# Performance work log

Measured on AMD Instinct MI355X. Metric: run time of the kernel, lower is better.

## Reference

```python
import jax, jax.numpy as jnp
from jax import lax
import numpy as np

H = 256  # hidden_size


def gru_last(x, Wih, Whh, bih, bhh):
    """Single-layer torch-convention GRU; returns last hidden state.
    x: [B, T, C] -> [B, H]"""
    B, T, _ = x.shape
    h_dim = Whh.shape[1]
    xW = x @ Wih.T + bih  # [B, T, 3H], precompute input gates
    def step(h, xw):
        gi_r, gi_z, gi_n = jnp.split(xw, 3, axis=-1)
        gh = h @ Whh.T + bhh
        gh_r, gh_z, gh_n = jnp.split(gh, 3, axis=-1)
        r = jax.nn.sigmoid(gi_r + gh_r)
        z = jax.nn.sigmoid(gi_z + gh_z)
        n = jnp.tanh(gi_n + r * gh_n)
        return (1.0 - z) * n + z * h, None
    h0 = jnp.zeros((B, h_dim), x.dtype)
    hT, _ = lax.scan(step, h0, jnp.swapaxes(xW, 0, 1))
    return hT


def setup_inputs() -> dict:
    key = jax.random.key(0)
    ks = jax.random.split(key, 16)
    B, N, M, C, C1 = 32, 64, 64, 64, 16
    inter = 2 * H + 6 * C + C1  # 912
    s = 0.05
    x1 = jax.random.normal(ks[0], (B, N, C1), jnp.float32)
    states = jax.random.normal(ks[1], (B, N, M, C), jnp.float32)
    perm1 = jax.vmap(lambda k: jax.random.permutation(k, M))(jax.random.split(ks[2], N)).astype(jnp.int64)
    perm2 = jax.vmap(lambda k: jax.random.permutation(k, N))(jax.random.split(ks[3], N)).astype(jnp.int64)
    return {
        "x1": x1, "states": states, "perm1": perm1, "perm2": perm2,
        # shared 2D->1D GRU (ModuleList([gru]*2) shares parameters)
        "gru2d_Wih": jax.random.normal(ks[4], (3 * H, C), jnp.float32) * s,
        "gru2d_Whh": jax.random.normal(ks[5], (3 * H, H), jnp.float32) * s,
        "gru2d_bih": jax.random.normal(ks[6], (3 * H,), jnp.float32) * s,
        "gru2d_bhh": jax.random.normal(ks[7], (3 * H,), jnp.float32) * s,
        "gru1d_Wih": jax.random.normal(ks[8], (3 * H, inter), jnp.float32) * s,
        "gru1d_Whh": jax.random.normal(ks[9], (3 * H, H), jnp.float32) * s,
        "gru1d_bih": jax.random.normal(ks[10], (3 * H,), jnp.float32) * s,
        "gru1d_bhh": jax.random.normal(ks[11], (3 * H,), jnp.float32) * s,
        "fc1_W": jax.random.normal(ks[12], (H, 3 * inter + H), jnp.float32) * s,
        "fc1_b": jax.random.normal(ks[13], (H,), jnp.float32) * s,
        "fc2_W": jax.random.normal(ks[14], (1, H), jnp.float32) * s,
        "fc2_b": jax.random.normal(ks[15], (1,), jnp.float32) * s,
    }


def reference(x1, states, perm1, perm2,
              gru2d_Wih, gru2d_Whh, gru2d_bih, gru2d_bhh,
              gru1d_Wih, gru1d_Whh, gru1d_bih, gru1d_bhh,
              fc1_W, fc1_b, fc2_W, fc2_b):
    B, N, M, C = states.shape
    d = [states.max(1), states.mean(1), states.min(1),   # [B, M, C] each (N==M)
         states.max(2), states.mean(2), states.min(2)]   # [B, N, C] each
    idx = jnp.arange(N)[:, None]
    # g1[b,i,t,c] = states[b, i, perm1[i,t], c]
    g1 = states[:, idx, perm1, :]                         # [B, N, M, C]
    # g2[b,i,t,c] = states[b, perm2[i,t], i, c]
    g2 = states[:, perm2, idx, :]                         # [B, N, N, C]
    sd1 = gru_last(g1.reshape(B * N, M, C), gru2d_Wih, gru2d_Whh, gru2d_bih, gru2d_bhh).reshape(B, N, H)
    sd2 = gru_last(g2.reshape(B * N, N, C), gru2d_Wih, gru2d_Whh, gru2d_bih, gru2d_bhh).reshape(B, N, H)
    f = jnp.concatenate(d + [sd1, sd2], axis=2)           # [B, N, 6C + 2H]
    f = jnp.concatenate([x1, f], axis=-1)                 # [B, N, inter]
    hlast = gru_last(f, gru1d_Wih, gru1d_Whh, gru1d_bih, gru1d_bhh)  # [B, H]
    g = jnp.concatenate([f.max(1), f.mean(1), f.min(1), hlast], axis=1)
    h = jax.nn.relu(g @ fc1_W.T + fc1_b)
    out = h @ fc2_W.T + fc2_b
    return out.reshape(B)
```

## Files before the change

kernel.cpp:

```cpp
#include <hip/hip_runtime.h>
#include <cmath>

#define B_ 32
#define N_ 64
#define H_ 256
#define G3_ 768
#define INTER_ 912
#define KP_ 928
#define FCIN_ 2992

#define PADA 264
#define PADX 72

typedef __attribute__((ext_vector_type(8))) short short8;
typedef __attribute__((ext_vector_type(4))) short sshort4;
typedef __attribute__((ext_vector_type(4))) float float4v;

#define MFMA __builtin_amdgcn_mfma_f32_16x16x32_bf16

__device__ __forceinline__ float sigmoid_f(float x) {
    return __builtin_amdgcn_rcpf(1.0f + __builtin_amdgcn_exp2f(-1.44269504f * x));
}
__device__ __forceinline__ float tanh_fast(float x) {
    return 1.0f - 2.0f * __builtin_amdgcn_rcpf(1.0f + __builtin_amdgcn_exp2f(2.88539008f * x));
}
__device__ __forceinline__ unsigned f2bf_bits(float x) {
    unsigned u = __float_as_uint(x);
    return (u + 0x7fffu + ((u >> 16) & 1u)) >> 16;
}
__device__ __forceinline__ short f2bf(float x) { return (short)f2bf_bits(x); }

__global__ __launch_bounds__(256) void prep_kernel(
        const float* __restrict__ Whh2, const float* __restrict__ Wih2,
        const float* __restrict__ Whh1, const float* __restrict__ Wih1,
        const float* __restrict__ fc1W,
        short* __restrict__ Bfrag, short* __restrict__ Bfrag1,
        short* __restrict__ Bfrag1W, float* __restrict__ fc1Wt) {
    int idx = blockIdx.x * 256 + threadIdx.x;
    if (idx < 10 * 48 * 64 * 8) {
        int j = idx & 7, lane = (idx >> 3) & 63, tile = idx >> 9;
        int nt = tile % 48, kt = tile / 48;
        int n = nt * 16 + (lane & 15);
        int kb = (lane >> 4) * 8 + j;
        float v = (kt < 8) ? Whh2[n * 256 + kt * 32 + kb]
                           : Wih2[n * 64 + (kt - 8) * 32 + kb];
        Bfrag[idx] = f2bf(v);
    }
    if (idx < 8 * 48 * 64 * 8) {
        int j = idx & 7, lane = (idx >> 3) & 63, tile = idx >> 9;
        int nt = tile % 48, kt = tile / 48;
        int n = nt * 16 + (lane & 15);
        int k = kt * 32 + (lane >> 4) * 8 + j;
        Bfrag1[idx] = f2bf(Whh1[n * 256 + k]);
    }
    if (idx < 29 * 48 * 64 * 8) {
        int j = idx & 7, lane = (idx >> 3) & 63, tile = idx >> 9;
        int nt = tile % 48, kt = tile / 48;
        int n = nt * 16 + (lane & 15);
        int k = kt * 32 + (lane >> 4) * 8 + j;
        Bfrag1W[idx] = (k < INTER_) ? f2bf(Wih1[n * INTER_ + k]) : (short)0;
    }
    if (idx < FCIN_ * 256) {
        int o = idx & 255, i = idx >> 8;
        fc1Wt[idx] = fc1W[o * FCIN_ + i];
    }
}

__global__ __launch_bounds__(256) void reduce_states_kernel(
        const float* __restrict__ states, const float* __restrict__ x1,
        float* __restrict__ f) {
    const int c = threadIdx.x & 63;
    const int bj = blockIdx.x * 4 + (threadIdx.x >> 6);
    const int b = bj >> 6, j = bj & 63;
    const float* p1 = states + b * 262144 + j * 64 + c;
    const float* p2 = states + b * 262144 + j * 4096 + c;
    float mx1 = -1e30f, mn1 = 1e30f, sm1 = 0.f;
    float mx2 = -1e30f, mn2 = 1e30f, sm2 = 0.f;
    #pragma unroll 8
    for (int n = 0; n < 64; ++n) {
        float v = p1[n * 4096];
        mx1 = fmaxf(mx1, v); mn1 = fminf(mn1, v); sm1 += v;
    }
    #pragma unroll 8
    for (int m = 0; m < 64; ++m) {
        float v = p2[m * 64];
        mx2 = fmaxf(mx2, v); mn2 = fminf(mn2, v); sm2 += v;
    }
    float* fr = f + bj * INTER_;
    fr[16 + c]  = mx1;  fr[80 + c]  = sm1 * (1.f / 64.f);  fr[144 + c] = mn1;
    fr[208 + c] = mx2;  fr[272 + c] = sm2 * (1.f / 64.f);  fr[336 + c] = mn2;
    if (c < 16) fr[c] = x1[bj * 16 + c];
}

__global__ __launch_bounds__(512, 1) void gru2d_mfma(
        const float* __restrict__ states,
        const int* __restrict__ perm1, const int* __restrict__ perm2,
        const short* __restrict__ Bfrag,
        const float* __restrict__ bih, const float* __restrict__ bhh,
        float* __restrict__ f) {
    __shared__ short hA[2][16 * PADA];
    __shared__ short xA[2][16 * PADX];
    __shared__ short8 Blds[2 * 48 * 64];
    __shared__ int perms[1024];

    const int tid = threadIdx.x;
    const int lane = tid & 63;
    const int w = tid >> 6;
    const int m = lane & 15;
    const int q = lane >> 4;
    const bool sd2 = blockIdx.x >= 128;
    const int sblock = (blockIdx.x & 127) * 16;

    for (int i = tid; i < 1024; i += 512) {
        int r = i >> 6, t = i & 63;
        int qq = (sblock + r) & 63;
        perms[i] = sd2 ? perm2[qq * 64 + t] : perm1[qq * 64 + t];
    }
    for (int i = tid; i < 16 * PADA; i += 512) hA[0][i] = 0;
    {
        const uint4* src = (const uint4*)(Bfrag + 6 * 48 * 64 * 8);
        uint4* dst = (uint4*)Blds;
        #pragma unroll
        for (int rep = 0; rep < 12; ++rep)
            dst[tid + rep * 512] = src[tid + rep * 512];
    }

    const short8* Bf8 = (const short8*)Bfrag;
    short8 Bres[36];
    #pragma unroll
    for (int kt = 0; kt < 6; ++kt)
        #pragma unroll
        for (int j = 0; j < 6; ++j)
            Bres[kt * 6 + j] = Bf8[(kt * 48 + 8 * j + w) * 64 + lane];

    const int u0 = 16 * w + m;
    const int u1 = 128 + u0;
    const float br0 = bih[u0] + bhh[u0],             br1 = bih[u1] + bhh[u1];
    const float bz0 = bih[256 + u0] + bhh[256 + u0], bz1 = bih[256 + u1] + bhh[256 + u1];
    const float bnx0 = bih[512 + u0], bnx1 = bih[512 + u1];
    const float bnh0 = bhh[512 + u0], bnh1 = bhh[512 + u1];

    float4v hreg0 = {0.f, 0.f, 0.f, 0.f}, hreg1 = {0.f, 0.f, 0.f, 0.f};

    {
        #pragma unroll
        for (int half = 0; half < 2; ++half) {
            int i = tid + half * 512;
            int r = i >> 6, c = i & 63;
            int s = sblock + r, b = s >> 6, qq = s & 63;
            int p = perms[r * 64 + 0];
            int src = sd2 ? ((b * 64 + p) * 64 + qq) * 64 + c
                          : ((b * 64 + qq) * 64 + p) * 64 + c;
            xA[0][r * PADX + c] = f2bf(states[src]);
        }
    }
    __syncthreads();

    for (int t = 0; t < 64; ++t) {
        const short* hAc = hA[t & 1];
        const short* xAc = xA[t & 1];

        short8 Bx[12];
        #pragma unroll
        for (int kt = 0; kt < 2; ++kt)
            #pragma unroll
            for (int j = 0; j < 6; ++j)
                Bx[kt * 6 + j] = Bf8[((8 + kt) * 48 + 8 * j + w) * 64 + lane];

        float xg0 = 0.f, xg1 = 0.f;
        int w0 = -1, w1 = -1;
        if (t + 1 < 64) {
            #pragma unroll
            for (int half = 0; half < 2; ++half) {
                int i = tid + half * 512;
                int r = i >> 6, c = i & 63;
                int s = sblock + r, b = s >> 6, qq = s & 63;
                int p = perms[r * 64 + t + 1];
                int src = sd2 ? ((b * 64 + p) * 64 + qq) * 64 + c
                              : ((b * 64 + qq) * 64 + p) * 64 + c;
                float v = states[src];
                if (half == 0) { xg0 = v; w0 = r * PADX + c; }
                else           { xg1 = v; w1 = r * PADX + c; }
            }
        }

        float4v aR0 = {br0, br0, br0, br0},     aR1 = {br1, br1, br1, br1};
        float4v aZ0 = {bz0, bz0, bz0, bz0},     aZ1 = {bz1, bz1, bz1, bz1};
        float4v aNh0 = {bnh0, bnh0, bnh0, bnh0}, aNh1 = {bnh1, bnh1, bnh1, bnh1};
        float4v aNx0 = {bnx0, bnx0, bnx0, bnx0}, aNx1 = {bnx1, bnx1, bnx1, bnx1};

        #pragma unroll
        for (int kt = 0; kt < 6; ++kt) {
            short8 a = *(const short8*)(hAc + m * PADA + kt * 32 + q * 8);
            aR0  = MFMA(a, Bres[kt * 6 + 0], aR0, 0, 0, 0);
            aR1  = MFMA(a, Bres[kt * 6 + 1], aR1, 0, 0, 0);
            aZ0  = MFMA(a, Bres[kt * 6 + 2], aZ0, 0, 0, 0);
            aZ1  = MFMA(a, Bres[kt * 6 + 3], aZ1, 0, 0, 0);
            aNh0 = MFMA(a, Bres[kt * 6 + 4], aNh0, 0, 0, 0);
            aNh1 = MFMA(a, Bres[kt * 6 + 5], aNh1, 0, 0, 0);
        }
        #pragma unroll
        for (int kt = 0; kt < 2; ++kt) {
            short8 a = *(const short8*)(hAc + m * PADA + (6 + kt) * 32 + q * 8);
            short8 b0 = Blds[(kt * 48 + 8 * 0 + w) * 64 + lane];
            short8 b1 = Blds[(kt * 48 + 8 * 1 + w) * 64 + lane];
            short8 b2 = Blds[(kt * 48 + 8 * 2 + w) * 64 + lane];
            short8 b3 = Blds[(kt * 48 + 8 * 3 + w) * 64 + lane];
            short8 b4 = Blds[(kt * 48 + 8 * 4 + w) * 64 + lane];
            short8 b5 = Blds[(kt * 48 + 8 * 5 + w) * 64 + lane];
            aR0  = MFMA(a, b0, aR0, 0, 0, 0);
            aR1  = MFMA(a, b1, aR1, 0, 0, 0);
            aZ0  = MFMA(a, b2, aZ0, 0, 0, 0);
            aZ1  = MFMA(a, b3, aZ1, 0, 0, 0);
            aNh0 = MFMA(a, b4, aNh0, 0, 0, 0);
            aNh1 = MFMA(a, b5, aNh1, 0, 0, 0);
        }
        #pragma unroll
        for (int kt = 0; kt < 2; ++kt) {
            short8 a = *(const short8*)(xAc + m * PADX + kt * 32 + q * 8);
            aR0  = MFMA(a, Bx[kt * 6 + 0], aR0, 0, 0, 0);
            aR1  = MFMA(a, Bx[kt * 6 + 1], aR1, 0, 0, 0);
            aZ0  = MFMA(a, Bx[kt * 6 + 2], aZ0, 0, 0, 0);
            aZ1  = MFMA(a, Bx[kt * 6 + 3], aZ1, 0, 0, 0);
            aNx0 = MFMA(a, Bx[kt * 6 + 4], aNx0, 0, 0, 0);
            aNx1 = MFMA(a, Bx[kt * 6 + 5], aNx1, 0, 0, 0);
        }

        short* hAn = hA[(t + 1) & 1];
        #pragma unroll
        for (int p = 0; p < 4; ++p) {
            int row = q * 4 + p;
            float r0 = sigmoid_f(aR0[p]);
            float z0 = sigmoid_f(aZ0[p]);
            float n0 = tanh_fast(aNx0[p] + r0 * aNh0[p]);
            float h0 = n0 + z0 * (hreg0[p] - n0);
            hreg0[p] = h0;
            hAn[row * PADA + u0] = f2bf(h0);
            float r1 = sigmoid_f(aR1[p]);
            float z1 = sigmoid_f(aZ1[p]);
            float n1 = tanh_fast(aNx1[p] + r1 * aNh1[p]);
            float h1 = n1 + z1 * (hreg1[p] - n1);
            hreg1[p] = h1;
            hAn[row * PADA + u1] = f2bf(h1);
        }
        if (t + 1 < 64) {
            xA[(t + 1) & 1][w0] = f2bf(xg0);
            xA[(t + 1) & 1][w1] = f2bf(xg1);
        }
        __syncthreads();
    }

    const int off = sd2 ? 656 : 400;
    #pragma unroll
    for (int p = 0; p < 4; ++p) {
        int s = sblock + q * 4 + p;
        f[s * INTER_ + off + u0] = hreg0[p];
        f[s * INTER_ + off + u1] = hreg1[p];
    }
}

__global__ __launch_bounds__(256) void convert_f_kernel(
        const float* __restrict__ f, short* __restrict__ fbf) {
    int idx = blockIdx.x * 256 + threadIdx.x;
    int row = idx / 232;
    int c4 = (idx - row * 232) * 4;
    if (row >= 2048) return;
    sshort4 o;
    if (c4 < INTER_) {
        float4v v = *(const float4v*)(f + row * INTER_ + c4);
        o[0] = f2bf(v[0]); o[1] = f2bf(v[1]); o[2] = f2bf(v[2]); o[3] = f2bf(v[3]);
    } else {
        o[0] = 0; o[1] = 0; o[2] = 0; o[3] = 0;
    }
    *(sshort4*)(fbf + row * KP_ + c4) = o;
}

__global__ __launch_bounds__(256) void gemm_xw1_mfma(
        const short* __restrict__ fbf, const short* __restrict__ BfragW,
        const float* __restrict__ bih, float* __restrict__ xw) {
    const int tid = threadIdx.x;
    const int lane = tid & 63;
    const int w = tid >> 6;
    const int m = lane & 15;
    const int q = lane >> 4;
    const int tn = blockIdx.x;
    const int tm = blockIdx.y;
    const int rowb = tm * 64 + w * 16;
    const short8* Bf8 = (const short8*)BfragW;

    float4v acc[4];
    #pragma unroll
    for (int nn = 0; nn < 4; ++nn) {
        float b = bih[tn * 64 + nn * 16 + m];
        acc[nn][0] = b; acc[nn][1] = b; acc[nn][2] = b; acc[nn][3] = b;
    }

    const short* arow = fbf + (rowb + m) * KP_;
    short8 a_cur = *(const short8*)(arow + q * 8);
    short8 b_cur[4];
    #pragma unroll
    for (int nn = 0; nn < 4; ++nn)
        b_cur[nn] = Bf8[(tn * 4 + nn) * 64 + lane];

    for (int kt = 0; kt < 29; ++kt) {
        short8 a_nxt = a_cur;
        short8 b_nxt[4];
        if (kt + 1 < 29) {
            a_nxt = *(const short8*)(arow + (kt + 1) * 32 + q * 8);
            #pragma unroll
            for (int nn = 0; nn < 4; ++nn)
                b_nxt[nn] = Bf8[((kt + 1) * 48 + tn * 4 + nn) * 64 + lane];
        }
        #pragma unroll
        for (int nn = 0; nn < 4; ++nn)
            acc[nn] = MFMA(a_cur, b_cur[nn], acc[nn], 0, 0, 0);
        a_cur = a_nxt;
        #pragma unroll
        for (int nn = 0; nn < 4; ++nn) b_cur[nn] = b_nxt[nn];
    }

    #pragma unroll
    for (int p = 0; p < 4; ++p) {
        int row = rowb + q * 4 + p;
        #pragma unroll
        for (int nn = 0; nn < 4; ++nn)
            xw[row * G3_ + tn * 64 + nn * 16 + m] = acc[nn][p];
    }
}

__global__ __launch_bounds__(512, 1) void gru1d_mfma(
        const float* __restrict__ xw, const short* __restrict__ Bfrag1,
        const float* __restrict__ bhh, float* __restrict__ hlast) {
    __shared__ short hA[2][16 * PADA];
    __shared__ short8 Blds[2 * 48 * 64];

    const int tid = threadIdx.x;
    const int lane = tid & 63;
    const int w = tid >> 6;
    const int m = lane & 15;
    const int q = lane >> 4;
    const int sblock = blockIdx.x * 16;

    for (int i = tid; i < 16 * PADA; i += 512) hA[0][i] = 0;
    {
        const uint4* src = (const uint4*)(Bfrag1 + 6 * 48 * 64 * 8);
        uint4* dst = (uint4*)Blds;
        #pragma unroll
        for (int rep = 0; rep < 12; ++rep)
            dst[tid + rep * 512] = src[tid + rep * 512];
    }
    const short8* Bf8 = (const short8*)Bfrag1;
    short8 Bres[36];
    #pragma unroll
    for (int kt = 0; kt < 6; ++kt)
        #pragma unroll
        for (int j = 0; j < 6; ++j)
            Bres[kt * 6 + j] = Bf8[(kt * 48 + 8 * j + w) * 64 + lane];

    const int u0 = 16 * w + m;
    const int u1 = 128 + u0;
    const float br0 = bhh[u0],       br1 = bhh[u1];
    const float bz0 = bhh[256 + u0], bz1 = bhh[256 + u1];
    const float bn0 = bhh[512 + u0], bn1 = bhh[512 + u1];

    float4v hreg0 = {0.f, 0.f, 0.f, 0.f}, hreg1 = {0.f, 0.f, 0.f, 0.f};
    __syncthreads();

    for (int t = 0; t < 64; ++t) {
        const short* hAc = hA[t & 1];

        float giR0[4], giR1[4], giZ0[4], giZ1[4], giN0[4], giN1[4];
        #pragma unroll
        for (int p = 0; p < 4; ++p) {
            const float* gr = xw + ((sblock + q * 4 + p) * 64 + t) * G3_;
            giR0[p] = gr[u0];        giR1[p] = gr[u1];
            giZ0[p] = gr[256 + u0];  giZ1[p] = gr[256 + u1];
            giN0[p] = gr[512 + u0];  giN1[p] = gr[512 + u1];
        }

        float4v aR0 = {br0, br0, br0, br0}, aR1 = {br1, br1, br1, br1};
        float4v aZ0 = {bz0, bz0, bz0, bz0}, aZ1 = {bz1, bz1, bz1, bz1};
        float4v aN0 = {bn0, bn0, bn0, bn0}, aN1 = {bn1, bn1, bn1, bn1};

        #pragma unroll
        for (int kt = 0; kt < 6; ++kt) {
            short8 a = *(const short8*)(hAc + m * PADA + kt * 32 + q * 8);
            aR0 = MFMA(a, Bres[kt * 6 + 0], aR0, 0, 0, 0);
            aR1 = MFMA(a, Bres[kt * 6 + 1], aR1, 0, 0, 0);
            aZ0 = MFMA(a, Bres[kt * 6 + 2], aZ0, 0, 0, 0);
            aZ1 = MFMA(a, Bres[kt * 6 + 3], aZ1, 0, 0, 0);
            aN0 = MFMA(a, Bres[kt * 6 + 4], aN0, 0, 0, 0);
            aN1 = MFMA(a, Bres[kt * 6 + 5], aN1, 0, 0, 0);
        }
        #pragma unroll
        for (int kt = 0; kt < 2; ++kt) {
            short8 a = *(const short8*)(hAc + m * PADA + (6 + kt) * 32 + q * 8);
            short8 b0 = Blds[(kt * 48 + 8 * 0 + w) * 64 + lane];
            short8 b1 = Blds[(kt * 48 + 8 * 1 + w) * 64 + lane];
            short8 b2 = Blds[(kt * 48 + 8 * 2 + w) * 64 + lane];
            short8 b3 = Blds[(kt * 48 + 8 * 3 + w) * 64 + lane];
            short8 b4 = Blds[(kt * 48 + 8 * 4 + w) * 64 + lane];
            short8 b5 = Blds[(kt * 48 + 8 * 5 + w) * 64 + lane];
            aR0 = MFMA(a, b0, aR0, 0, 0, 0);
            aR1 = MFMA(a, b1, aR1, 0, 0, 0);
            aZ0 = MFMA(a, b2, aZ0, 0, 0, 0);
            aZ1 = MFMA(a, b3, aZ1, 0, 0, 0);
            aN0 = MFMA(a, b4, aN0, 0, 0, 0);
            aN1 = MFMA(a, b5, aN1, 0, 0, 0);
        }

        short* hAn = hA[(t + 1) & 1];
        #pragma unroll
        for (int p = 0; p < 4; ++p) {
            int row = q * 4 + p;
            float r0 = sigmoid_f(giR0[p] + aR0[p]);
            float z0 = sigmoid_f(giZ0[p] + aZ0[p]);
            float n0 = tanh_fast(giN0[p] + r0 * aN0[p]);
            float h0 = n0 + z0 * (hreg0[p] - n0);
            hreg0[p] = h0;
            hAn[row * PADA + u0] = f2bf(h0);
            float r1 = sigmoid_f(giR1[p] + aR1[p]);
            float z1 = sigmoid_f(giZ1[p] + aZ1[p]);
            float n1 = tanh_fast(giN1[p] + r1 * aN1[p]);
            float h1 = n1 + z1 * (hreg1[p] - n1);
            hreg1[p] = h1;
            hAn[row * PADA + u1] = f2bf(h1);
        }
        __syncthreads();
    }

    #pragma unroll
    for (int p = 0; p < 4; ++p) {
        int s = sblock + q * 4 + p;
        hlast[s * 256 + u0] = hreg0[p];
        hlast[s * 256 + u1] = hreg1[p];
    }
}

__global__ __launch_bounds__(256) void tail_kernel(
        const float* __restrict__ f, const float* __restrict__ hlast,
        const float* __restrict__ fc1Wt, const float* __restrict__ fc1b,
        const float* __restrict__ fc2W, const float* __restrict__ fc2b,
        float* __restrict__ out) {
    __shared__ float g_lds[FCIN_];
    __shared__ float red[256];
    const int tid = threadIdx.x;
    const int b = blockIdx.x;
    for (int i = tid; i < INTER_; i += 256) {
        float mx = -1e30f, mn = 1e30f, sm = 0.f;
        for (int t = 0; t < 64; ++t) {
            float v = f[(b * 64 + t) * INTER_ + i];
            mx = fmaxf(mx, v); mn = fminf(mn, v); sm += v;
        }
        g_lds[i] = mx;
        g_lds[INTER_ + i] = sm * (1.f / 64.f);
        g_lds[2 * INTER_ + i] = mn;
    }
    g_lds[3 * INTER_ + tid] = hlast[b * 256 + tid];
    __syncthreads();
    float acc = fc1b[tid];
    for (int i = 0; i < FCIN_; ++i)
        acc = fmaf(g_lds[i], fc1Wt[i * 256 + tid], acc);
    float hv = fmaxf(acc, 0.f);
    red[tid] = hv * fc2W[tid];
    __syncthreads();
    if (tid == 0) {
        float s = fc2b[0];
        for (int i = 0; i < 256; ++i) s += red[i];
        out[b] = s;
    }
}

extern "C" void kernel_launch(void* const* d_in, const int* in_sizes, int n_in,
                              void* d_out, int out_size, void* d_ws, size_t ws_size,
                              hipStream_t stream) {
    const float* x1     = (const float*)d_in[0];
    const float* states = (const float*)d_in[1];
    const int*   perm1  = (const int*)d_in[2];
    const int*   perm2  = (const int*)d_in[3];
    const float* Wih2   = (const float*)d_in[4];
    const float* Whh2   = (const float*)d_in[5];
    const float* bih2   = (const float*)d_in[6];
    const float* bhh2   = (const float*)d_in[7];
    const float* Wih1   = (const float*)d_in[8];
    const float* Whh1   = (const float*)d_in[9];
    const float* bih1   = (const float*)d_in[10];
    const float* bhh1   = (const float*)d_in[11];
    const float* fc1W   = (const float*)d_in[12];
    const float* fc1b   = (const float*)d_in[13];
    const float* fc2W   = (const float*)d_in[14];
    const float* fc2b   = (const float*)d_in[15];
    float* out = (float*)d_out;

    float* ws = (float*)d_ws;
    short* Bfrag   = (short*)ws;
    short* Bfrag1  = (short*)(ws + 122880);
    short* Bfrag1W = (short*)(ws + 122880 + 98304);
    float* fc1Wt   = ws + 577536;
    float* f       = fc1Wt + FCIN_ * 256;
    short* fbf     = (short*)(f + 2048 * INTER_);
    float* xw1     = f + 2048 * INTER_ + 950272;
    float* hlast   = xw1 + 2048 * G3_;

    prep_kernel<<<dim3(2992), 256, 0, stream>>>(Whh2, Wih2, Whh1, Wih1, fc1W,
                                                Bfrag, Bfrag1, Bfrag1W, fc1Wt);
    reduce_states_kernel<<<dim3(512), 256, 0, stream>>>(states, x1, f);
    gru2d_mfma<<<dim3(256), 512, 0, stream>>>(states, perm1, perm2, Bfrag,
                                              bih2, bhh2, f);
    convert_f_kernel<<<dim3(1856), 256, 0, stream>>>(f, fbf);
    gemm_xw1_mfma<<<dim3(12, 32), 256, 0, stream>>>(fbf, Bfrag1W, bih1, xw1);
    gru1d_mfma<<<dim3(2), 512, 0, stream>>>(xw1, Bfrag1, bhh1, hlast);
    tail_kernel<<<dim3(32), 256, 0, stream>>>(f, hlast, fc1Wt, fc1b, fc2W, fc2b, out);
}
```

Before: 632.6 us.

## Overlap f reductions with gru1d, hoist Bx loads, transpose xw layout

Moves the per-batch max/mean/min reduction over f out of the tail kernel and into 32 extra blocks of the gru1d launch, so it runs concurrently with the two-block serial recurrence. The xw1 output is stored time-major so each gru1d step reads a contiguous slab. It also hoists the loop-invariant Bx weight fragments out of the gru2d time loop, uses nontemporal loads in the reductions, splits the fc1 dot product into four accumulators, and replaces the serial final sum with a wave shuffle reduction. Keeping Bx resident adds register pressure in gru2d, and the four-way accumulation changes floating-point summation order slightly.

```diff
diff --git a/kernel.cpp b/kernel.cpp
--- a/kernel.cpp
+++ b/kernel.cpp
@@ -8,6 +8,7 @@
 #define INTER_ 912
 #define KP_ 928
 #define FCIN_ 2992
+#define GRED_ 2736
 
 #define PADA 264
 #define PADX 72
@@ -78,12 +79,12 @@
     float mx2 = -1e30f, mn2 = 1e30f, sm2 = 0.f;
     #pragma unroll 8
     for (int n = 0; n < 64; ++n) {
-        float v = p1[n * 4096];
+        float v = __builtin_nontemporal_load(p1 + n * 4096);
         mx1 = fmaxf(mx1, v); mn1 = fminf(mn1, v); sm1 += v;
     }
     #pragma unroll 8
     for (int m = 0; m < 64; ++m) {
-        float v = p2[m * 64];
+        float v = __builtin_nontemporal_load(p2 + m * 64);
         mx2 = fmaxf(mx2, v); mn2 = fminf(mn2, v); sm2 += v;
     }
     float* fr = f + bj * INTER_;
@@ -133,6 +134,13 @@
         for (int j = 0; j < 6; ++j)
             Bres[kt * 6 + j] = Bf8[(kt * 48 + 8 * j + w) * 64 + lane];
 
+    short8 Bx[12];
+    #pragma unroll
+    for (int kt = 0; kt < 2; ++kt)
+        #pragma unroll
+        for (int j = 0; j < 6; ++j)
+            Bx[kt * 6 + j] = Bf8[((8 + kt) * 48 + 8 * j + w) * 64 + lane];
+
     const int u0 = 16 * w + m;
     const int u1 = 128 + u0;
     const float br0 = bih[u0] + bhh[u0],             br1 = bih[u1] + bhh[u1];
@@ -159,13 +167,6 @@
     for (int t = 0; t < 64; ++t) {
         const short* hAc = hA[t & 1];
         const short* xAc = xA[t & 1];
-
-        short8 Bx[12];
-        #pragma unroll
-        for (int kt = 0; kt < 2; ++kt)
-            #pragma unroll
-            for (int j = 0; j < 6; ++j)
-                Bx[kt * 6 + j] = Bf8[((8 + kt) * 48 + 8 * j + w) * 64 + lane];
 
         float xg0 = 0.f, xg1 = 0.f;
         int w0 = -1, w1 = -1;
@@ -322,19 +323,39 @@
     #pragma unroll
     for (int p = 0; p < 4; ++p) {
         int row = rowb + q * 4 + p;
+        int seq = row >> 6, t = row & 63;
         #pragma unroll
         for (int nn = 0; nn < 4; ++nn)
-            xw[row * G3_ + tn * 64 + nn * 16 + m] = acc[nn][p];
-    }
-}
-
-__global__ __launch_bounds__(512, 1) void gru1d_mfma(
+            xw[(t * 32 + seq) * G3_ + tn * 64 + nn * 16 + m] = acc[nn][p];
+    }
+}
+
+__global__ __launch_bounds__(512, 1) void gru1d_freduce(
         const float* __restrict__ xw, const short* __restrict__ Bfrag1,
-        const float* __restrict__ bhh, float* __restrict__ hlast) {
+        const float* __restrict__ bhh, float* __restrict__ hlast,
+        const float* __restrict__ f, float* __restrict__ g) {
     __shared__ short hA[2][16 * PADA];
     __shared__ short8 Blds[2 * 48 * 64];
 
     const int tid = threadIdx.x;
+
+    if (blockIdx.x >= 2) {
+        const int b = blockIdx.x - 2;
+        for (int i = tid; i < INTER_; i += 512) {
+            const float* fp = f + (size_t)(b * 64) * INTER_ + i;
+            float mx = -1e30f, mn = 1e30f, sm = 0.f;
+            #pragma unroll 8
+            for (int t = 0; t < 64; ++t) {
+                float v = __builtin_nontemporal_load(fp + t * INTER_);
+                mx = fmaxf(mx, v); mn = fminf(mn, v); sm += v;
+            }
+            g[b * GRED_ + i] = mx;
+            g[b * GRED_ + INTER_ + i] = sm * (1.f / 64.f);
+            g[b * GRED_ + 2 * INTER_ + i] = mn;
+        }
+        return;
+    }
+
     const int lane = tid & 63;
     const int w = tid >> 6;
     const int m = lane & 15;
@@ -372,7 +393,7 @@
         float giR0[4], giR1[4], giZ0[4], giZ1[4], giN0[4], giN1[4];
         #pragma unroll
         for (int p = 0; p < 4; ++p) {
-            const float* gr = xw + ((sblock + q * 4 + p) * 64 + t) * G3_;
+            const float* gr = xw + (size_t)(t * 32 + sblock + q * 4 + p) * G3_;
             giR0[p] = gr[u0];        giR1[p] = gr[u1];
             giZ0[p] = gr[256 + u0];  giZ1[p] = gr[256 + u1];
             giN0[p] = gr[512 + u0];  giN1[p] = gr[512 + u1];
@@ -437,38 +458,36 @@
     }
 }
 
-__global__ __launch_bounds__(256) void tail_kernel(
-        const float* __restrict__ f, const float* __restrict__ hlast,
+__global__ __launch_bounds__(256) void tail_fc(
+        const float* __restrict__ g, const float* __restrict__ hlast,
         const float* __restrict__ fc1Wt, const float* __restrict__ fc1b,
         const float* __restrict__ fc2W, const float* __restrict__ fc2b,
         float* __restrict__ out) {
     __shared__ float g_lds[FCIN_];
-    __shared__ float red[256];
+    __shared__ float red[4];
     const int tid = threadIdx.x;
     const int b = blockIdx.x;
-    for (int i = tid; i < INTER_; i += 256) {
-        float mx = -1e30f, mn = 1e30f, sm = 0.f;
-        for (int t = 0; t < 64; ++t) {
-            float v = f[(b * 64 + t) * INTER_ + i];
-            mx = fmaxf(mx, v); mn = fminf(mn, v); sm += v;
-        }
-        g_lds[i] = mx;
-        g_lds[INTER_ + i] = sm * (1.f / 64.f);
-        g_lds[2 * INTER_ + i] = mn;
-    }
-    g_lds[3 * INTER_ + tid] = hlast[b * 256 + tid];
+    for (int i = tid; i < GRED_; i += 256) g_lds[i] = g[b * GRED_ + i];
+    g_lds[GRED_ + tid] = hlast[b * 256 + tid];
     __syncthreads();
-    float acc = fc1b[tid];
-    for (int i = 0; i < FCIN_; ++i)
-        acc = fmaf(g_lds[i], fc1Wt[i * 256 + tid], acc);
+
+    float a0 = 0.f, a1 = 0.f, a2 = 0.f, a3 = 0.f;
+    for (int i = 0; i < FCIN_; i += 4) {
+        a0 = fmaf(g_lds[i],     fc1Wt[(i) * 256 + tid],     a0);
+        a1 = fmaf(g_lds[i + 1], fc1Wt[(i + 1) * 256 + tid], a1);
+        a2 = fmaf(g_lds[i + 2], fc1Wt[(i + 2) * 256 + tid], a2);
+        a3 = fmaf(g_lds[i + 3], fc1Wt[(i + 3) * 256 + tid], a3);
+    }
+    float acc = ((a0 + a1) + (a2 + a3)) + fc1b[tid];
     float hv = fmaxf(acc, 0.f);
-    red[tid] = hv * fc2W[tid];
+    float part = hv * fc2W[tid];
+    #pragma unroll
+    for (int off = 32; off >= 1; off >>= 1)
+        part += __shfl_down(part, off, 64);
+    if ((tid & 63) == 0) red[tid >> 6] = part;
     __syncthreads();
-    if (tid == 0) {
-        float s = fc2b[0];
-        for (int i = 0; i < 256; ++i) s += red[i];
-        out[b] = s;
-    }
+    if (tid == 0)
+        out[b] = fc2b[0] + red[0] + red[1] + red[2] + red[3];
 }
 
 extern "C" void kernel_launch(void* const* d_in, const int* in_sizes, int n_in,
@@ -501,6 +520,7 @@
     short* fbf     = (short*)(f + 2048 * INTER_);
     float* xw1     = f + 2048 * INTER_ + 950272;
     float* hlast   = xw1 + 2048 * G3_;
+    float* g       = hlast + 8192;
 
     prep_kernel<<<dim3(2992), 256, 0, stream>>>(Whh2, Wih2, Whh1, Wih1, fc1W,
                                                 Bfrag, Bfrag1, Bfrag1W, fc1Wt);
@@ -509,6 +529,6 @@
                                               bih2, bhh2, f);
     convert_f_kernel<<<dim3(1856), 256, 0, stream>>>(f, fbf);
     gemm_xw1_mfma<<<dim3(12, 32), 256, 0, stream>>>(fbf, Bfrag1W, bih1, xw1);
-    gru1d_mfma<<<dim3(2), 512, 0, stream>>>(xw1, Bfrag1, bhh1, hlast);
-    tail_kernel<<<dim3(32), 256, 0, stream>>>(f, hlast, fc1Wt, fc1b, fc2W, fc2b, out);
-}
+    gru1d_freduce<<<dim3(34), 512, 0, stream>>>(xw1, Bfrag1, bhh1, hlast, f, g);
+    tail_fc<<<dim3(32), 256, 0, stream>>>(g, hlast, fc1Wt, fc1b, fc2W, fc2b, out);
+}
```

New measurement: 637.1 us. Within noise of the previous version (+0.7%).
